# Performance work log

Hardware: AMD Instinct MI355X
Metric: run time of the kernel (lower is better)

Reference implementation:

```python
import jax, jax.numpy as jnp
import numpy as np

N, E, T, F = 20000, 320000, 64, 16
HG, HT = 128, 256


def setup_inputs() -> dict:
    key = jax.random.key(0)
    ks = jax.random.split(key, 18)
    s = 0.05
    p = lambda k, shape: jax.random.normal(k, shape, jnp.float32) * s
    return {
        "x_seq": jax.random.normal(ks[0], (1, T, N, F), jnp.float32),
        "edge_index": jax.random.randint(ks[1], (2, E), 0, N, jnp.int32),
        # SAGEConv 1 (PyG default: mean aggregation; lin_l on aggregated neighbors w/ bias, lin_r on root w/o bias)
        "W1l": p(ks[2], (HG, F)), "b1l": p(ks[3], (HG,)), "W1r": p(ks[4], (HG, F)),
        # SAGEConv 2
        "W2l": p(ks[5], (HG, HG)), "b2l": p(ks[6], (HG,)), "W2r": p(ks[7], (HG, HG)),
        # GRU (torch gate order: r, z, n)
        "W_ih": p(ks[8], (3 * HT, HG)), "W_hh": p(ks[9], (3 * HT, HT)),
        "b_ih": p(ks[10], (3 * HT,)), "b_hh": p(ks[11], (3 * HT,)),
        # head: Linear(HT,64) -> ReLU -> Linear(64,1)
        "Wh1": p(ks[12], (64, HT)), "bh1": p(ks[13], (64,)),
        "Wh2": p(ks[14], (1, 64)), "bh2": p(ks[15], (1,)),
    }


def reference(x_seq, edge_index, W1l, b1l, W1r, W2l, b2l, W2r,
              W_ih, W_hh, b_ih, b_hh, Wh1, bh1, Wh2, bh2):
    n_nodes = x_seq.shape[2]
    src, dst = edge_index[0], edge_index[1]
    # in-degree for mean aggregation (0 -> output 0, matching scatter-mean)
    deg = jax.ops.segment_sum(jnp.ones(src.shape[0], x_seq.dtype), dst,
                              num_segments=n_nodes)
    inv_deg = jnp.where(deg > 0, 1.0 / deg, 0.0)[:, None]  # [N,1]

    def sage(x, Wl, bl, Wr):
        # mean over incoming neighbor messages, then linear + root linear
        agg = jax.ops.segment_sum(x[src], dst, num_segments=n_nodes) * inv_deg
        return agg @ Wl.T + bl + x @ Wr.T

    def graph_step(carry, x_t):  # x_t: [N, F]
        h = jax.nn.relu(sage(x_t, W1l, b1l, W1r))
        h = jax.nn.relu(sage(h, W2l, b2l, W2r))
        return carry, h.mean(axis=0)  # [HG]

    _, Hg = jax.lax.scan(graph_step, 0, x_seq[0])  # [T, HG]

    hidden_t = W_hh.shape[1]

    def gru_step(h, x_t):
        gi = x_t @ W_ih.T + b_ih
        gh = h @ W_hh.T + b_hh
        i_r, i_z, i_n = jnp.split(gi, 3)
        h_r, h_z, h_n = jnp.split(gh, 3)
        r = jax.nn.sigmoid(i_r + h_r)
        z = jax.nn.sigmoid(i_z + h_z)
        n = jnp.tanh(i_n + r * h_n)
        h_new = (1.0 - z) * n + z * h
        return h_new, h_new

    h0 = jnp.zeros((hidden_t,), x_seq.dtype)
    h_last, _ = jax.lax.scan(gru_step, h0, Hg)  # [HT]

    y = jax.nn.relu(h_last @ Wh1.T + bh1) @ Wh2.T + bh2  # [1]
    return y
```

## Files before the change

### kernel.cpp

```cpp
#include <hip/hip_runtime.h>
#include <hip/hip_bf16.h>

#define N_NODES 20000
#define N_EDGES 320000
#define T_STEPS 64
#define F_IN    16
#define HGd     128
#define HTd     256
#define INVN    (1.0f/20000.0f)
#define NTILES   625
#define S1T      79
#define NG64     313
#define QX       32.0f
#define INVQX    (1.0f/32.0f)
#define S_HALF   ((N_NODES + 1) * HGd)

typedef __attribute__((ext_vector_type(8))) short short8;
typedef __attribute__((ext_vector_type(4))) float f32x4;
typedef __attribute__((ext_vector_type(2))) float f32x2;
typedef __attribute__((ext_vector_type(2))) _Float16 half2t;

static __device__ __forceinline__ ushort f2bf(float f) {
    __hip_bfloat16 b = __float2bfloat16(f);
    return *reinterpret_cast<ushort*>(&b);
}
static __device__ __forceinline__ half2t u2h(uint u) {
    half2t h; __builtin_memcpy(&h, &u, 4); return h;
}
static __device__ __forceinline__ uint h2u(half2t h) {
    uint u; __builtin_memcpy(&u, &h, 4); return u;
}
static __device__ __forceinline__ uint packf16(float a, float b) {
    auto h = __builtin_amdgcn_cvt_pkrtz(a, b);
    uint u; __builtin_memcpy(&u, &h, 4); return u;
}
static __device__ __forceinline__ ushort f2h(float a) {
    return (ushort)(packf16(a, a) & 0xffffu);
}

__global__ void k_zero(int* __restrict__ deg, float* __restrict__ HgP,
                       int* __restrict__ jobc, int* __restrict__ bins,
                       uint* __restrict__ h1f, int tch) {
    int i = blockIdx.x * blockDim.x + threadIdx.x;
    if (i < N_NODES) deg[i] = 0;
    if (i < T_STEPS * 8 * HGd) HgP[i] = 0.0f;
    if (i < 1024) jobc[i] = 0;
    if (i < 256) bins[i] = 0;
    if (i < tch * 64) {
        int sl = i >> 6, j = i & 63;
        h1f[(size_t)sl * (S_HALF / 2) + (size_t)N_NODES * (HGd / 2) + j] = 0u;
    }
}

__global__ void k_degree(const int* __restrict__ ei, int* __restrict__ deg) {
    int e = blockIdx.x * blockDim.x + threadIdx.x;
    if (e < N_EDGES) atomicAdd(&deg[ei[N_EDGES + e]], 1);
}

__global__ __launch_bounds__(1024) void k_scan(const int* __restrict__ deg,
        int* __restrict__ rp, int* __restrict__ cursor, float* __restrict__ invd) {
    __shared__ int sh[1024];
    __shared__ int carry_s;
    int tid = threadIdx.x;
    if (tid == 0) { carry_s = 0; rp[0] = 0; }
    __syncthreads();
    for (int base = 0; base < N_NODES; base += 1024) {
        int i = base + tid;
        int v = (i < N_NODES) ? deg[i] : 0;
        sh[tid] = v;
        __syncthreads();
        for (int off = 1; off < 1024; off <<= 1) {
            int t = (tid >= off) ? sh[tid - off] : 0;
            __syncthreads();
            sh[tid] += t;
            __syncthreads();
        }
        int inc = sh[tid] + carry_s;
        if (i < N_NODES) {
            rp[i + 1] = inc;
            cursor[i] = inc - v;
            invd[i] = (v > 0) ? (1.0f / (float)v) : 0.0f;
        }
        __syncthreads();
        if (tid == 1023) carry_s = inc;
        __syncthreads();
    }
}

__global__ void k_fill(const int* __restrict__ ei, int* __restrict__ cursor,
                       int* __restrict__ csr) {
    int e = blockIdx.x * blockDim.x + threadIdx.x;
    if (e < N_EDGES) {
        int d = ei[N_EDGES + e];
        int p = atomicAdd(&cursor[d], 1);
        csr[p] = ei[e];
    }
}

__global__ void k_hist(const int* __restrict__ deg, int* __restrict__ bins) {
    int i = blockIdx.x * blockDim.x + threadIdx.x;
    if (i < N_NODES) atomicAdd(&bins[min(deg[i], 255)], 1);
}

__global__ __launch_bounds__(256) void k_binscan(const int* __restrict__ bins,
        int* __restrict__ bincur, int* __restrict__ nodebefore,
        int* __restrict__ edgebefore, int* __restrict__ edgebp, int* __restrict__ rp2p) {
    __shared__ int sh[256], she[256], shp[256];
    int tid = threadIdx.x;
    int b = bins[tid];
    int dp = (tid + 7) & ~7;
    sh[tid] = b;
    she[tid] = b * tid;
    shp[tid] = b * dp;
    __syncthreads();
    for (int off = 1; off < 256; off <<= 1) {
        int v = (tid >= off) ? sh[tid - off] : 0;
        int ve = (tid >= off) ? she[tid - off] : 0;
        int vp = (tid >= off) ? shp[tid - off] : 0;
        __syncthreads();
        sh[tid] += v; she[tid] += ve; shp[tid] += vp;
        __syncthreads();
    }
    bincur[tid] = sh[tid] - b;
    nodebefore[tid] = sh[tid] - b;
    edgebefore[tid] = she[tid] - b * tid;
    edgebp[tid] = shp[tid] - b * dp;
    if (tid == 255) rp2p[N_NODES] = shp[255];
}

__global__ void k_perm(const int* __restrict__ deg, int* __restrict__ bincur,
                       const int* __restrict__ nodebefore, const int* __restrict__ edgebefore,
                       const int* __restrict__ edgebp, const float* __restrict__ invd,
                       int* __restrict__ perm, int* __restrict__ pos,
                       int* __restrict__ rp2, float* __restrict__ invd2,
                       int* __restrict__ degs2, int* __restrict__ rp2p) {
    int i = blockIdx.x * blockDim.x + threadIdx.x;
    if (i < N_NODES) {
        int d = min(deg[i], 255);
        int p = atomicAdd(&bincur[d], 1);
        int rank = p - nodebefore[d];
        perm[p] = i;
        pos[i] = p;
        rp2[p] = edgebefore[d] + rank * d;
        rp2p[p] = edgebp[d] + rank * ((d + 7) & ~7);
        invd2[p] = invd[i];
        degs2[p] = deg[i];
        if (i == 0) rp2[N_NODES] = N_EDGES;
    }
}

__global__ void k_csr2(const int* __restrict__ rp, const int* __restrict__ pos,
                       const int* __restrict__ rp2, const int* __restrict__ csr,
                       int* __restrict__ csr2) {
    int i = blockIdx.x * blockDim.x + threadIdx.x;
    if (i < N_NODES) {
        int s = rp[i], e = rp[i + 1];
        int o = rp2[pos[i]];
        for (int k = s; k < e; ++k) csr2[o + (k - s)] = csr[k];
    }
}

__global__ void k_csr2p(const int* __restrict__ rp, const int* __restrict__ pos,
                        const int* __restrict__ rp2p, const int* __restrict__ csr,
                        int* __restrict__ csr2p) {
    int i = blockIdx.x * blockDim.x + threadIdx.x;
    if (i < N_NODES) {
        int s = rp[i], d = rp[i + 1] - s;
        int dp = (d + 7) & ~7;
        int o = rp2p[pos[i]];
        for (int k = 0; k < d; ++k) csr2p[o + k] = csr[s + k];
        for (int k = d; k < dp; ++k) csr2p[o + k] = N_NODES;
    }
}

__global__ __launch_bounds__(512) void k_tb(const int* __restrict__ rp2, int* __restrict__ tb) {
    __shared__ int sh[512];
    int t = threadIdx.x;
    int md = 0;
    if (t < NG64 && t * 64 < N_NODES) {
        int last = min((t + 1) * 64, N_NODES) - 1;
        md = rp2[last + 1] - rp2[last];
    }
    sh[t] = 64 * md;
    __syncthreads();
    for (int off = 1; off < 512; off <<= 1) {
        int v = (t >= off) ? sh[t - off] : 0;
        __syncthreads();
        sh[t] += v;
        __syncthreads();
    }
    tb[t + 1] = sh[t];
    if (t == 0) tb[0] = 0;
}

__global__ void k_csr3(const int* __restrict__ rp2, const int* __restrict__ tb,
                       const int* __restrict__ csr2, int* __restrict__ csr3) {
    int p = blockIdx.x * blockDim.x + threadIdx.x;
    if (p < N_NODES) {
        int s = rp2[p], d = rp2[p + 1] - s;
        int base = tb[p >> 6];
        int lane = p & 63;
        for (int j = 0; j < d; ++j) csr3[base + j * 64 + lane] = csr2[s + j];
    }
}

__global__ void k_qx(const float* __restrict__ xs, int* __restrict__ x8, int n4) {
    int i = blockIdx.x * blockDim.x + threadIdx.x;
    if (i < n4) {
        float4 v = reinterpret_cast<const float4*>(xs)[i];
        int q8 = __builtin_amdgcn_cvt_pk_fp8_f32(v.x * QX, v.y * QX, 0, false);
        q8 = __builtin_amdgcn_cvt_pk_fp8_f32(v.z * QX, v.w * QX, q8, true);
        x8[i] = q8;
    }
}

__global__ void k_prepw(const float* __restrict__ W1l, const float* __restrict__ W1r,
                        const float* __restrict__ W2l, const float* __restrict__ W2r,
                        const float* __restrict__ W_ih, const float* __restrict__ W_hh,
                        ushort* __restrict__ W1T2, ushort* __restrict__ WT2f,
                        float* __restrict__ WihT, uint* __restrict__ W_hhq) {
    int i = blockIdx.x * blockDim.x + threadIdx.x;
    const int n1 = 128 * 32, n2 = 128 * 256, n3 = 128 * 768, n4 = 128 * 768;
    if (i < n1) {
        int o = i >> 5, k = i & 31;
        float v = (k < 16) ? W1l[o * 16 + k] : W1r[o * 16 + (k - 16)];
        W1T2[i] = f2bf(v);
    } else if (i < n1 + n2) {
        int j = i - n1; int o = j >> 8, k = j & 255;
        float v = (k < 128) ? W2l[o * 128 + k] : W2r[o * 128 + (k - 128)];
        WT2f[j] = f2h(v);
    } else if (i < n1 + n2 + n3) {
        int j = i - n1 - n2; int k = j / 768, g = j % 768;
        WihT[j] = W_ih[g * 128 + k];
    } else if (i < n1 + n2 + n3 + n4) {
        int j = i - n1 - n2 - n3; int dw = j / 768, row = j % 768;
        float a = W_hh[(size_t)row * HTd + 2 * dw];
        float b = W_hh[(size_t)row * HTd + 2 * dw + 1];
        W_hhq[j] = packf16(a, b);
    }
}

__global__ __launch_bounds__(256) void k_sage1(
        const char* __restrict__ x8_, const int* __restrict__ tb,
        const int* __restrict__ csr3, const int* __restrict__ degs2,
        const float* __restrict__ invd2,
        const ushort* __restrict__ W1T2, const float* __restrict__ b1l,
        const int* __restrict__ perm, ushort* __restrict__ h1f_,
        int* __restrict__ jobc, int C) {
    __shared__ ushort u[256 * 40];
    __shared__ int pnode[256];
    __shared__ int job_s;
    int tid = threadIdx.x;
    int l = tid & 63, w = tid >> 6;
    int lane15 = l & 15, g4 = l >> 4;
    const int xcd = blockIdx.x & 7;
    const int cmin = (C < 8) ? C : 8;
    const int ci = xcd % cmin;
    const int reps = (C >= 8) ? (C >> 3) : 1;
    int* ctr = jobc + ci;
    const int njobs = reps * S1T;

    short8 bfr1[2];
    float bb1[2];
#pragma unroll
    for (int ct = 0; ct < 2; ++ct) {
        int o16 = w * 32 + ct * 16 + lane15;
        bfr1[ct] = *reinterpret_cast<const short8*>(W1T2 + o16 * 32 + g4 * 8);
        bb1[ct] = b1l[o16];
    }

    for (;;) {
        if (tid == 0) job_s = atomicAdd(ctr, 1);
        __syncthreads();
        int job = job_s;
        if (job >= njobs) break;
        int rep = job / S1T;
        int tile = job - rep * S1T;
        int tl = ci + (rep << 3);
        const char* xq = x8_ + (size_t)tl * N_NODES * F_IN;
        ushort* h1f = h1f_ + (size_t)tl * S_HALF;
        int p = tile * 256 + tid;
        int node = (p < N_NODES) ? perm[p] : -1;
        pnode[tid] = node;

        float acc[16];
#pragma unroll
        for (int k = 0; k < 16; ++k) acc[k] = 0.0f;
        float rootv[16];
#pragma unroll
        for (int k = 0; k < 16; ++k) rootv[k] = 0.0f;
        if (node >= 0) {
            int d = degs2[p];
            const int base = tb[p >> 6] + (p & 63);
            for (int j = 0; j < d; ++j) {
                int idx = csr3[base + j * 64];
                uint4 row = *reinterpret_cast<const uint4*>(xq + (size_t)idx * F_IN);
#pragma unroll
                for (int c = 0; c < 4; ++c) {
                    uint vd = c == 0 ? row.x : c == 1 ? row.y : c == 2 ? row.z : row.w;
                    f32x2 lo = __builtin_amdgcn_cvt_pk_f32_fp8((int)vd, false);
                    f32x2 hi = __builtin_amdgcn_cvt_pk_f32_fp8((int)vd, true);
                    acc[4 * c + 0] += lo.x; acc[4 * c + 1] += lo.y;
                    acc[4 * c + 2] += hi.x; acc[4 * c + 3] += hi.y;
                }
            }
            float id = invd2[p] * INVQX;
#pragma unroll
            for (int k = 0; k < 16; ++k) acc[k] *= id;
            uint4 rv = *reinterpret_cast<const uint4*>(xq + (size_t)node * F_IN);
#pragma unroll
            for (int c = 0; c < 4; ++c) {
                uint vd = c == 0 ? rv.x : c == 1 ? rv.y : c == 2 ? rv.z : rv.w;
                f32x2 lo = __builtin_amdgcn_cvt_pk_f32_fp8((int)vd, false);
                f32x2 hi = __builtin_amdgcn_cvt_pk_f32_fp8((int)vd, true);
                rootv[4 * c + 0] = lo.x * INVQX; rootv[4 * c + 1] = lo.y * INVQX;
                rootv[4 * c + 2] = hi.x * INVQX; rootv[4 * c + 3] = hi.y * INVQX;
            }
        }
        {
            uint dw[16];
#pragma unroll
            for (int i = 0; i < 8; ++i)
                dw[i] = (uint)f2bf(acc[2 * i]) | ((uint)f2bf(acc[2 * i + 1]) << 16);
#pragma unroll
            for (int i = 0; i < 8; ++i)
                dw[8 + i] = (uint)f2bf(rootv[2 * i]) | ((uint)f2bf(rootv[2 * i + 1]) << 16);
            ushort* ur = u + tid * 40;
#pragma unroll
            for (int c = 0; c < 4; ++c)
                *reinterpret_cast<uint4*>(ur + c * 8) =
                    make_uint4(dw[4 * c], dw[4 * c + 1], dw[4 * c + 2], dw[4 * c + 3]);
        }
        __syncthreads();

#pragma unroll 4
        for (int rt = 0; rt < 16; ++rt) {
            int row = rt * 16 + lane15;
            short8 af = *reinterpret_cast<const short8*>(u + row * 40 + g4 * 8);
            f32x4 a0 = __builtin_amdgcn_mfma_f32_16x16x32_bf16(af, bfr1[0], (f32x4)(0.0f), 0, 0, 0);
            f32x4 a1 = __builtin_amdgcn_mfma_f32_16x16x32_bf16(af, bfr1[1], (f32x4)(0.0f), 0, 0, 0);
#pragma unroll
            for (int j = 0; j < 4; ++j) {
                int nl = rt * 16 + g4 * 4 + j;
                int nd = pnode[nl];
                if (nd >= 0) {
                    float v0 = fmaxf(a0[j] + bb1[0], 0.0f);
                    float v1 = fmaxf(a1[j] + bb1[1], 0.0f);
                    h1f[(size_t)nd * HGd + w * 32 + lane15] = f2h(v0);
                    h1f[(size_t)nd * HGd + w * 32 + 16 + lane15] = f2h(v1);
                }
            }
        }
    }
}

__global__ __launch_bounds__(256) void k_sage2(
        const ushort* __restrict__ h1f_,
        const int* __restrict__ rp2p, const int* __restrict__ csr2p,
        const float* __restrict__ invd2,
        const ushort* __restrict__ WT2f, const float* __restrict__ b2l,
        const int* __restrict__ perm, float* __restrict__ HgP,
        int* __restrict__ jobc, int t0, int C) {
    __shared__ uint4 usm4[32 * 512 / 16];
    __shared__ int pnode[32];
    __shared__ int job_s;
    char* ub = (char*)usm4;
    int tid = threadIdx.x;
    int l = tid & 63, w = tid >> 6;
    int lane15 = l & 15, g4 = l >> 4;
    const int xcd = blockIdx.x & 7;
    const int cmin = (C < 8) ? C : 8;
    const int ci = xcd % cmin;
    const int reps = (C >= 8) ? (C >> 3) : 1;
    int* ctr = jobc + ci;
    const int njobs = reps * NTILES;

    short8 bfr[2][8];
    float bb[2];
#pragma unroll
    for (int ct = 0; ct < 2; ++ct) {
        int n = w * 32 + ct * 16 + lane15;
        const ushort* bp = WT2f + n * 256 + g4 * 8;
#pragma unroll
        for (int ks = 0; ks < 8; ++ks)
            bfr[ct][ks] = *reinterpret_cast<const short8*>(bp + ks * 32);
        bb[ct] = b2l[n];
    }

    for (;;) {
        if (tid == 0) job_s = atomicAdd(ctr, 1);
        __syncthreads();
        int job = job_s;
        if (job >= njobs) break;
        int rep = job / NTILES;
        int tile = job - rep * NTILES;
        int tl = ci + ((reps - 1 - rep) << 3);
        int t = t0 + tl;
        const ushort* h1f = h1f_ + (size_t)tl * S_HALF;
        int nbase = tile * 32;
        if (tid < 32) pnode[tid] = perm[nbase + tid];
        __syncthreads();

        for (int i = tid; i < 512; i += 256) {
            int nl = i >> 4, seg = i & 15;
            uint4 v = *reinterpret_cast<const uint4*>(h1f + (size_t)pnode[nl] * HGd + seg * 8);
            *reinterpret_cast<uint4*>(ub + ((nl * 1024 / 2 + 256 + seg * 16) ^ ((nl & 7) << 4))) = v;
        }

#pragma unroll
        for (int g = 0; g < 2; ++g) {
            int nl = w * 8 + g * 4 + g4;
            int sl = rp2p[nbase + nl];
            int dp = rp2p[nbase + nl + 1] - sl;
            const int* cp = csr2p + sl;
            half2t a0 = (half2t)0, a1 = (half2t)0, a2 = (half2t)0, a3 = (half2t)0;
            if (dp > 0) {
                int idx[8];
#pragma unroll
                for (int uu = 0; uu < 8; ++uu) idx[uu] = cp[uu];
                for (int j = 0; j < dp; j += 8) {
                    uint4 vv[8];
#pragma unroll
                    for (int uu = 0; uu < 8; ++uu)
                        vv[uu] = *reinterpret_cast<const uint4*>(h1f + (size_t)idx[uu] * HGd + lane15 * 8);
                    cp += 8;
#pragma unroll
                    for (int uu = 0; uu < 8; ++uu) idx[uu] = cp[uu];
#pragma unroll
                    for (int uu = 0; uu < 8; ++uu) {
                        a0 += u2h(vv[uu].x);
                        a1 += u2h(vv[uu].y);
                        a2 += u2h(vv[uu].z);
                        a3 += u2h(vv[uu].w);
                    }
                }
            }
            float id = invd2[nbase + nl];
            _Float16 idh = (_Float16)id;
            half2t idv; idv[0] = idh; idv[1] = idh;
            uint4 pk;
            pk.x = h2u(a0 * idv);
            pk.y = h2u(a1 * idv);
            pk.z = h2u(a2 * idv);
            pk.w = h2u(a3 * idv);
            *reinterpret_cast<uint4*>(ub + ((nl * 512 + lane15 * 16) ^ ((nl & 7) << 4))) = pk;
        }
        __syncthreads();

        f32x4 acc[2][2];
#pragma unroll
        for (int rt = 0; rt < 2; ++rt)
#pragma unroll
            for (int ct = 0; ct < 2; ++ct) acc[rt][ct] = (f32x4)(0.0f);

#pragma unroll
        for (int ks = 0; ks < 8; ++ks) {
#pragma unroll
            for (int rt = 0; rt < 2; ++rt) {
                int row = rt * 16 + lane15;
                int byt = (row * 512 + (ks * 32 + g4 * 8) * 2) ^ ((row & 7) << 4);
                short8 af = *reinterpret_cast<const short8*>(ub + byt);
                acc[rt][0] = __builtin_amdgcn_mfma_f32_16x16x32_f16(af, bfr[0][ks], acc[rt][0], 0, 0, 0);
                acc[rt][1] = __builtin_amdgcn_mfma_f32_16x16x32_f16(af, bfr[1][ks], acc[rt][1], 0, 0, 0);
            }
        }

#pragma unroll
        for (int ct = 0; ct < 2; ++ct) {
            float sum = 0.f;
#pragma unroll
            for (int rt = 0; rt < 2; ++rt)
#pragma unroll
                for (int j = 0; j < 4; ++j)
                    sum += fmaxf(acc[rt][ct][j] + bb[ct], 0.f);
            sum += __shfl_xor(sum, 16);
            sum += __shfl_xor(sum, 32);
            if (g4 == 0) {
                int n = w * 32 + ct * 16 + lane15;
                atomicAdd(&HgP[(t * 8 + (job & 7)) * HGd + n], sum);
            }
        }
    }
}

__global__ __launch_bounds__(768) void k_gi(const float* __restrict__ HgP,
        const float* __restrict__ WihT, const float* __restrict__ b_ih,
        float* __restrict__ gi_all) {
    __shared__ float x[HGd];
    int t = blockIdx.x, g = threadIdx.x;
    if (g < HGd) {
        float s = 0.f;
#pragma unroll
        for (int p = 0; p < 8; ++p) s += HgP[(t * 8 + p) * HGd + g];
        x[g] = s * INVN;
    }
    __syncthreads();
    float a = b_ih[g];
    for (int k = 0; k < HGd; ++k) a += WihT[k * 768 + g] * x[k];
    gi_all[t * 768 + g] = a;
}

__global__ __launch_bounds__(768, 3) void k_gru1b(const float* __restrict__ gi_all,
        const uint* __restrict__ W_hhq, const float* __restrict__ b_hh,
        const float* __restrict__ Wh1, const float* __restrict__ bh1,
        const float* __restrict__ Wh2, const float* __restrict__ bh2,
        float* __restrict__ out) {
    int tid = threadIdx.x;
    uint wv[128];
#pragma unroll
    for (int i = 0; i < 128; ++i) wv[i] = W_hhq[i * 768 + tid];
    float bh = b_hh[tid];

    __shared__ float hs[HTd];
    __shared__ uint h2s[HTd / 2];
    __shared__ float gh[3 * HTd];
    if (tid < HTd) hs[tid] = 0.0f;
    if (tid < HTd / 2) h2s[tid] = 0u;
    __syncthreads();

    for (int t = 0; t < T_STEPS; ++t) {
        float s = bh;
#pragma unroll
        for (int i = 0; i < 128; i += 4) {
            uint4 hh = *reinterpret_cast<const uint4*>(&h2s[i]);
            s = __builtin_amdgcn_fdot2(u2h(wv[i + 0]), u2h(hh.x), s, false);
            s = __builtin_amdgcn_fdot2(u2h(wv[i + 1]), u2h(hh.y), s, false);
            s = __builtin_amdgcn_fdot2(u2h(wv[i + 2]), u2h(hh.z), s, false);
            s = __builtin_amdgcn_fdot2(u2h(wv[i + 3]), u2h(hh.w), s, false);
        }
        gh[tid] = s;
        __syncthreads();
        if (tid < HTd) {
            float gir = gi_all[t * 768 + tid];
            float giz = gi_all[t * 768 + HTd + tid];
            float gin = gi_all[t * 768 + 2 * HTd + tid];
            float r = 1.0f / (1.0f + expf(-(gir + gh[tid])));
            float z = 1.0f / (1.0f + expf(-(giz + gh[HTd + tid])));
            float n = tanhf(gin + r * gh[2 * HTd + tid]);
            hs[tid] = (1.0f - z) * n + z * hs[tid];
        }
        __syncthreads();
        if (tid < HTd / 2)
            h2s[tid] = packf16(hs[2 * tid], hs[2 * tid + 1]);
        __syncthreads();
    }

    __shared__ float act[64];
    if (tid < 64) {
        float a = bh1[tid];
        const float* wr = Wh1 + tid * HTd;
        for (int k = 0; k < HTd; k += 4) {
            float4 wv4 = *reinterpret_cast<const float4*>(wr + k);
            a += wv4.x * hs[k] + wv4.y * hs[k + 1] + wv4.z * hs[k + 2] + wv4.w * hs[k + 3];
        }
        act[tid] = fmaxf(a, 0.0f);
    }
    __syncthreads();
    if (tid == 0) {
        float y = bh2[0];
        for (int j = 0; j < 64; ++j) y += Wh2[j] * act[j];
        out[0] = y;
    }
}

extern "C" void kernel_launch(void* const* d_in, const int* in_sizes, int n_in,
                              void* d_out, int out_size, void* d_ws, size_t ws_size,
                              hipStream_t stream) {
    const float* x_seq = (const float*)d_in[0];
    const int*   ei    = (const int*)d_in[1];
    const float* W1l   = (const float*)d_in[2];
    const float* b1l   = (const float*)d_in[3];
    const float* W1r   = (const float*)d_in[4];
    const float* W2l   = (const float*)d_in[5];
    const float* b2l   = (const float*)d_in[6];
    const float* W2r   = (const float*)d_in[7];
    const float* W_ih  = (const float*)d_in[8];
    const float* W_hh  = (const float*)d_in[9];
    const float* b_ih  = (const float*)d_in[10];
    const float* b_hh  = (const float*)d_in[11];
    const float* Wh1   = (const float*)d_in[12];
    const float* bh1   = (const float*)d_in[13];
    const float* Wh2   = (const float*)d_in[14];
    const float* bh2   = (const float*)d_in[15];
    float* out = (float*)d_out;

    char* ws = (char*)d_ws;
    size_t off = 0;
    auto take = [&](size_t nbytes) -> void* {
        void* p = (void*)(ws + off);
        off += (nbytes + 255) & ~(size_t)255;
        return p;
    };
    int*    deg    = (int*)take(N_NODES * 4);
    int*    rp     = (int*)take((N_NODES + 1) * 4);
    int*    cursor = (int*)take(N_NODES * 4);
    int*    csr    = (int*)take(N_EDGES * 4);
    float*  invd   = (float*)take(N_NODES * 4);
    int*    perm   = (int*)take(N_NODES * 4);
    int*    pos    = (int*)take(N_NODES * 4);
    int*    rp2    = (int*)take((N_NODES + 2) * 4);
    int*    rp2p   = (int*)take((N_NODES + 2) * 4);
    int*    csr2   = (int*)take(N_EDGES * 4);
    int*    csr2p  = (int*)take(480100 * 4);
    float*  invd2  = (float*)take(N_NODES * 4);
    int*    degs2  = (int*)take(N_NODES * 4);
    int*    tb     = (int*)take(520 * 4);
    int*    csr3   = (int*)take(360000 * 4);
    int*    bins   = (int*)take(256 * 4);
    int*    bincur = (int*)take(256 * 4);
    int*    nodeb  = (int*)take(256 * 4);
    int*    edgeb  = (int*)take(256 * 4);
    int*    edgebp = (int*)take(256 * 4);
    ushort* W1T2   = (ushort*)take(128 * 32 * 2);
    ushort* WT2f   = (ushort*)take(128 * 256 * 2);
    float*  WihT   = (float*)take(128 * 768 * 4);
    uint*   W_hhq  = (uint*)take(128 * 768 * 4);
    float*  HgP    = (float*)take(T_STEPS * 8 * HGd * 4);
    float*  gi_all = (float*)take(T_STEPS * 768 * 4);
    int*    jobc   = (int*)take(1024 * 4);

    const size_t slice_h = (size_t)S_HALF * 2;
    const size_t slice_x = ((size_t)N_NODES * F_IN + 255) & ~(size_t)255;
    int T_CH = 64;
    while (T_CH > 1 && off + (size_t)T_CH * (slice_h + slice_x) > ws_size)
        T_CH >>= 1;
    ushort* h1f = (ushort*)take((size_t)T_CH * slice_h);
    char*   x8  = (char*)take((size_t)T_CH * slice_x);

    k_zero<<<256, 256, 0, stream>>>(deg, HgP, jobc, bins, (uint*)h1f, T_CH);
    k_degree<<<(N_EDGES + 255) / 256, 256, 0, stream>>>(ei, deg);
    k_scan<<<1, 1024, 0, stream>>>(deg, rp, cursor, invd);
    k_fill<<<(N_EDGES + 255) / 256, 256, 0, stream>>>(ei, cursor, csr);
    k_hist<<<(N_NODES + 255) / 256, 256, 0, stream>>>(deg, bins);
    k_binscan<<<1, 256, 0, stream>>>(bins, bincur, nodeb, edgeb, edgebp, rp2p);
    k_perm<<<(N_NODES + 255) / 256, 256, 0, stream>>>(deg, bincur, nodeb, edgeb, edgebp,
                                                      invd, perm, pos, rp2, invd2, degs2, rp2p);
    k_csr2<<<(N_NODES + 255) / 256, 256, 0, stream>>>(rp, pos, rp2, csr, csr2);
    k_csr2p<<<(N_NODES + 255) / 256, 256, 0, stream>>>(rp, pos, rp2p, csr, csr2p);
    k_tb<<<1, 512, 0, stream>>>(rp2, tb);
    k_csr3<<<(N_NODES + 255) / 256, 256, 0, stream>>>(rp2, tb, csr2, csr3);
    {
        int total = 128 * 32 + 128 * 256 + 128 * 768 + 128 * 768;
        k_prepw<<<(total + 255) / 256, 256, 0, stream>>>(W1l, W1r, W2l, W2r, W_ih, W_hh,
                                                         W1T2, WT2f, WihT, W_hhq);
    }
    int chunk = 0;
    for (int t0 = 0; t0 < T_STEPS; t0 += T_CH, ++chunk) {
        int C = T_CH;
        int n4 = C * N_NODES * F_IN / 4;
        k_qx<<<(n4 + 255) / 256, 256, 0, stream>>>(
            x_seq + (size_t)t0 * N_NODES * F_IN, (int*)x8, n4);
        k_sage1<<<2048, 256, 0, stream>>>(x8, tb, csr3, degs2, invd2, W1T2, b1l, perm,
                                          h1f, jobc + chunk * 16, C);
        k_sage2<<<2048, 256, 0, stream>>>(h1f, rp2p, csr2p, invd2, WT2f, b2l, perm, HgP,
                                          jobc + chunk * 16 + 8, t0, C);
    }
    k_gi<<<T_STEPS, 768, 0, stream>>>(HgP, WihT, b_ih, gi_all);
    k_gru1b<<<1, 768, 0, stream>>>(gi_all, W_hhq, b_hh, Wh1, bh1, Wh2, bh2, out);
}
```

Before: 1.123 ms.

## Build permuted CSR layouts with edge-parallel copy and process time in smaller chunks

Replaces three node-parallel CSR rebuild kernels, which serialize over each node's edges, with one edge-parallel kernel and a small padding kernel. The edge kernel binary-searches the row pointer to find each edge's node and writes directly into both the transposed sage1 layout and the padded sage2 layout, so the intermediate csr2 buffer is no longer needed. The time-chunk size drops from 64 to 16, which should keep the h1 and x8 working set closer to cache at the cost of more kernel launches. The HgP partial-sum slot is now keyed by tile instead of job index, and the job-counter stride is widened.

```diff
diff --git a/kernel.cpp b/kernel.cpp
--- a/kernel.cpp
+++ b/kernel.cpp
@@ -149,30 +149,6 @@
     }
 }
 
-__global__ void k_csr2(const int* __restrict__ rp, const int* __restrict__ pos,
-                       const int* __restrict__ rp2, const int* __restrict__ csr,
-                       int* __restrict__ csr2) {
-    int i = blockIdx.x * blockDim.x + threadIdx.x;
-    if (i < N_NODES) {
-        int s = rp[i], e = rp[i + 1];
-        int o = rp2[pos[i]];
-        for (int k = s; k < e; ++k) csr2[o + (k - s)] = csr[k];
-    }
-}
-
-__global__ void k_csr2p(const int* __restrict__ rp, const int* __restrict__ pos,
-                        const int* __restrict__ rp2p, const int* __restrict__ csr,
-                        int* __restrict__ csr2p) {
-    int i = blockIdx.x * blockDim.x + threadIdx.x;
-    if (i < N_NODES) {
-        int s = rp[i], d = rp[i + 1] - s;
-        int dp = (d + 7) & ~7;
-        int o = rp2p[pos[i]];
-        for (int k = 0; k < d; ++k) csr2p[o + k] = csr[s + k];
-        for (int k = d; k < dp; ++k) csr2p[o + k] = N_NODES;
-    }
-}
-
 __global__ __launch_bounds__(512) void k_tb(const int* __restrict__ rp2, int* __restrict__ tb) {
     __shared__ int sh[512];
     int t = threadIdx.x;
@@ -193,14 +169,35 @@
     if (t == 0) tb[0] = 0;
 }
 
-__global__ void k_csr3(const int* __restrict__ rp2, const int* __restrict__ tb,
-                       const int* __restrict__ csr2, int* __restrict__ csr3) {
-    int p = blockIdx.x * blockDim.x + threadIdx.x;
-    if (p < N_NODES) {
-        int s = rp2[p], d = rp2[p + 1] - s;
-        int base = tb[p >> 6];
-        int lane = p & 63;
-        for (int j = 0; j < d; ++j) csr3[base + j * 64 + lane] = csr2[s + j];
+__global__ void k_ecopy(const int* __restrict__ rp, const int* __restrict__ pos,
+                        const int* __restrict__ rp2p, const int* __restrict__ tb,
+                        const int* __restrict__ csr,
+                        int* __restrict__ csr3, int* __restrict__ csr2p) {
+    int e = blockIdx.x * blockDim.x + threadIdx.x;
+    if (e < N_EDGES) {
+        int lo = 0, hi = N_NODES - 1;
+#pragma unroll
+        for (int it = 0; it < 15; ++it) {
+            int mid = (lo + hi + 1) >> 1;
+            if (rp[mid] <= e) lo = mid; else hi = mid - 1;
+        }
+        int i = lo;
+        int j = e - rp[i];
+        int p = pos[i];
+        int v = csr[e];
+        csr3[tb[p >> 6] + j * 64 + (p & 63)] = v;
+        csr2p[rp2p[p] + j] = v;
+    }
+}
+
+__global__ void k_pad(const int* __restrict__ rp, const int* __restrict__ pos,
+                      const int* __restrict__ rp2p, int* __restrict__ csr2p) {
+    int i = blockIdx.x * blockDim.x + threadIdx.x;
+    if (i < N_NODES) {
+        int d = rp[i + 1] - rp[i];
+        int dp = (d + 7) & ~7;
+        int o = rp2p[pos[i]];
+        for (int k = d; k < dp; ++k) csr2p[o + k] = N_NODES;
     }
 }
 
@@ -283,12 +280,9 @@
         int node = (p < N_NODES) ? perm[p] : -1;
         pnode[tid] = node;
 
-        float acc[16];
-#pragma unroll
-        for (int k = 0; k < 16; ++k) acc[k] = 0.0f;
-        float rootv[16];
-#pragma unroll
-        for (int k = 0; k < 16; ++k) rootv[k] = 0.0f;
+        float acc[16], rootv[16];
+#pragma unroll
+        for (int k = 0; k < 16; ++k) { acc[k] = 0.0f; rootv[k] = 0.0f; }
         if (node >= 0) {
             int d = degs2[p];
             const int base = tb[p >> 6] + (p & 63);
@@ -404,7 +398,7 @@
         for (int i = tid; i < 512; i += 256) {
             int nl = i >> 4, seg = i & 15;
             uint4 v = *reinterpret_cast<const uint4*>(h1f + (size_t)pnode[nl] * HGd + seg * 8);
-            *reinterpret_cast<uint4*>(ub + ((nl * 1024 / 2 + 256 + seg * 16) ^ ((nl & 7) << 4))) = v;
+            *reinterpret_cast<uint4*>(ub + ((nl * 512 + 256 + seg * 16) ^ ((nl & 7) << 4))) = v;
         }
 
 #pragma unroll
@@ -452,7 +446,6 @@
         for (int rt = 0; rt < 2; ++rt)
 #pragma unroll
             for (int ct = 0; ct < 2; ++ct) acc[rt][ct] = (f32x4)(0.0f);
-
 #pragma unroll
         for (int ks = 0; ks < 8; ++ks) {
 #pragma unroll
@@ -464,7 +457,6 @@
                 acc[rt][1] = __builtin_amdgcn_mfma_f32_16x16x32_f16(af, bfr[1][ks], acc[rt][1], 0, 0, 0);
             }
         }
-
 #pragma unroll
         for (int ct = 0; ct < 2; ++ct) {
             float sum = 0.f;
@@ -477,7 +469,7 @@
             sum += __shfl_xor(sum, 32);
             if (g4 == 0) {
                 int n = w * 32 + ct * 16 + lane15;
-                atomicAdd(&HgP[(t * 8 + (job & 7)) * HGd + n], sum);
+                atomicAdd(&HgP[(t * 8 + (tile & 7)) * HGd + n], sum);
             }
         }
     }
@@ -600,8 +592,7 @@
     int*    pos    = (int*)take(N_NODES * 4);
     int*    rp2    = (int*)take((N_NODES + 2) * 4);
     int*    rp2p   = (int*)take((N_NODES + 2) * 4);
-    int*    csr2   = (int*)take(N_EDGES * 4);
-    int*    csr2p  = (int*)take(480100 * 4);
+    int*    csr2p  = (int*)take(480200 * 4);
     float*  invd2  = (float*)take(N_NODES * 4);
     int*    degs2  = (int*)take(N_NODES * 4);
     int*    tb     = (int*)take(520 * 4);
@@ -621,7 +612,7 @@
 
     const size_t slice_h = (size_t)S_HALF * 2;
     const size_t slice_x = ((size_t)N_NODES * F_IN + 255) & ~(size_t)255;
-    int T_CH = 64;
+    int T_CH = 16;
     while (T_CH > 1 && off + (size_t)T_CH * (slice_h + slice_x) > ws_size)
         T_CH >>= 1;
     ushort* h1f = (ushort*)take((size_t)T_CH * slice_h);
@@ -635,10 +626,9 @@
     k_binscan<<<1, 256, 0, stream>>>(bins, bincur, nodeb, edgeb, edgebp, rp2p);
     k_perm<<<(N_NODES + 255) / 256, 256, 0, stream>>>(deg, bincur, nodeb, edgeb, edgebp,
                                                       invd, perm, pos, rp2, invd2, degs2, rp2p);
-    k_csr2<<<(N_NODES + 255) / 256, 256, 0, stream>>>(rp, pos, rp2, csr, csr2);
-    k_csr2p<<<(N_NODES + 255) / 256, 256, 0, stream>>>(rp, pos, rp2p, csr, csr2p);
     k_tb<<<1, 512, 0, stream>>>(rp2, tb);
-    k_csr3<<<(N_NODES + 255) / 256, 256, 0, stream>>>(rp2, tb, csr2, csr3);
+    k_ecopy<<<(N_EDGES + 255) / 256, 256, 0, stream>>>(rp, pos, rp2p, tb, csr, csr3, csr2p);
+    k_pad<<<(N_NODES + 255) / 256, 256, 0, stream>>>(rp, pos, rp2p, csr2p);
     {
         int total = 128 * 32 + 128 * 256 + 128 * 768 + 128 * 768;
         k_prepw<<<(total + 255) / 256, 256, 0, stream>>>(W1l, W1r, W2l, W2r, W_ih, W_hh,
@@ -651,9 +641,9 @@
         k_qx<<<(n4 + 255) / 256, 256, 0, stream>>>(
             x_seq + (size_t)t0 * N_NODES * F_IN, (int*)x8, n4);
         k_sage1<<<2048, 256, 0, stream>>>(x8, tb, csr3, degs2, invd2, W1T2, b1l, perm,
-                                          h1f, jobc + chunk * 16, C);
+                                          h1f, jobc + chunk * 32, C);
         k_sage2<<<2048, 256, 0, stream>>>(h1f, rp2p, csr2p, invd2, WT2f, b2l, perm, HgP,
-                                          jobc + chunk * 16 + 8, t0, C);
+                                          jobc + chunk * 32 + 16, t0, C);
     }
     k_gi<<<T_STEPS, 768, 0, stream>>>(HgP, WihT, b_ih, gi_all);
     k_gru1b<<<1, 768, 0, stream>>>(gi_all, W_hhq, b_hh, Wh1, bh1, Wh2, bh2, out);
```

Result: slower. 1.267 ms (+12.9%).
